# Kernel tuning notes

Hardware: AMD Instinct MI355X
Metric: run time of the kernel (lower is better)

## Reference

```python
import jax, jax.numpy as jnp
import numpy as np

BATCH, IN_F, OUT_F, BASIS = 64, 512, 512, 8


def _cheb_basis(x):
    # Chebyshev basis T_k(tanh(x)) for k=1..BASIS; x: (b, i) -> (b, i, BASIS)
    theta = jnp.arccos(jnp.clip(jnp.tanh(x), -1.0 + 1e-6, 1.0 - 1e-6))
    ks = jnp.arange(1, BASIS + 1, dtype=x.dtype)
    return jnp.cos(theta[..., None] * ks)


def setup_inputs() -> dict:
    key = jax.random.key(0)
    k1, k2, k3 = jax.random.split(key, 3)
    x = jax.random.normal(k1, (BATCH, IN_F), dtype=jnp.float32)
    # xavier_normal_ on w: std = sqrt(2 / (fan_in + fan_out))
    w = jax.random.normal(k2, (IN_F, OUT_F), dtype=jnp.float32) * np.sqrt(2.0 / (IN_F + OUT_F))
    # normal_(c, 0, 0.1)
    c = jax.random.normal(k3, (IN_F, OUT_F, BASIS), dtype=jnp.float32) * 0.1
    return {"x": x, "w": w, "c": c}


def reference(x, w, c):
    # basis: (b, i, k); contract basis dim with c: (i, o, k) -> (b, i, o)
    basis = _cheb_basis(x)
    s = jnp.einsum("bik,iok->bio", basis, c)
    # residual SiLU(x) broadcast over o, weight by w, reduce over in_features
    out = jnp.einsum("bio,io->bo", jax.nn.silu(x)[:, :, None] + s, w)
    return out
```

## Files before the change

kernel.cpp:

```cpp
#include <hip/hip_runtime.h>

#define BATCH 64
#define IN_F 512
#define OUT_F 512
#define ICH 16
#define NKB (IN_F / ICH)
#define NNB 16

typedef short short8 __attribute__((ext_vector_type(8)));
typedef float f32x4 __attribute__((ext_vector_type(4)));

static __device__ __forceinline__ unsigned bfpk(float a, float b) {
    unsigned ua = __float_as_uint(a) + 0x8000u;
    unsigned ub = __float_as_uint(b) + 0x8000u;
    return __builtin_amdgcn_perm(ub, ua, 0x07060302u);
}

__global__ __launch_bounds__(256, 2) void kan_mfma(const float* __restrict__ x,
                                                   const float* __restrict__ w,
                                                   const float* __restrict__ c,
                                                   float* __restrict__ out) {
    __shared__ __align__(16) short T_lds[ICH * BATCH * 8];
    __shared__ __align__(16) short S_lds[BATCH * ICH];

    int nb  = blockIdx.x & (NNB - 1);
    int kb  = blockIdx.x >> 4;
    int i0  = kb * ICH;
    int o0  = nb * 32;
    int tid = threadIdx.x;

    {
        int b  = tid & 63;
        int wq = tid >> 6;
        float4 xv4 = *(const float4*)(x + (size_t)b * IN_F + i0 + wq * 4);
        float xs[4] = {xv4.x, xv4.y, xv4.z, xv4.w};
#pragma unroll
        for (int j = 0; j < 4; ++j) {
            int il = wq * 4 + j;
            float xv = xs[j];
            float xc = fminf(fmaxf(xv, -15.f), 15.f);
            float u  = __expf(-xc);
            float sl = __fdividef(xv, 1.0f + u);
            float u2 = u * u;
            float t  = __fdividef(1.0f - u2, 1.0f + u2);
            t = fminf(fmaxf(t, -1.0f + 1e-6f), 1.0f - 1e-6f);
            float t2 = t + t;
            float T1 = t;
            float T2 = fmaf(t2, T1, -1.0f);
            float T3 = fmaf(t2, T2, -T1);
            float T4 = fmaf(t2, T3, -T2);
            float T5 = fmaf(t2, T4, -T3);
            float T6 = fmaf(t2, T5, -T4);
            float T7 = fmaf(t2, T6, -T5);
            float T8 = fmaf(t2, T7, -T6);
            union { short8 v; unsigned u4[4]; } fr;
            fr.u4[0] = bfpk(T1, T2);
            fr.u4[1] = bfpk(T3, T4);
            fr.u4[2] = bfpk(T5, T6);
            fr.u4[3] = bfpk(T7, T8);
            *(short8*)&T_lds[(il * BATCH + b) * 8] = fr.v;
            S_lds[b * ICH + il] = (short)(bfpk(sl, 0.f) & 0xffffu);
        }
    }
    __syncthreads();

    int lane = tid & 63;
    int wid  = tid >> 6;
    int m    = lane & 15;
    int quad = lane >> 4;
    int oh   = wid & 1;
    int bp   = wid >> 1;
    int o    = o0 + oh * 16 + m;

    short8 af[2][4];
    short8 aw[2];
#pragma unroll
    for (int u = 0; u < 2; ++u) {
        int b = bp * 32 + u * 16 + m;
#pragma unroll
        for (int s = 0; s < 4; ++s)
            af[u][s] = *(const short8*)&T_lds[((s * 4 + quad) * BATCH + b) * 8];
        aw[u] = (quad < 2) ? *(const short8*)&S_lds[b * ICH + quad * 8]
                           : short8{0, 0, 0, 0, 0, 0, 0, 0};
    }

    f32x4 acc0 = {0.f, 0.f, 0.f, 0.f};
    f32x4 acc1 = {0.f, 0.f, 0.f, 0.f};

#pragma unroll
    for (int s = 0; s < 4; ++s) {
        int i = i0 + s * 4 + quad;
        const float4* cp = (const float4*)(c + ((size_t)i * OUT_F + o) * 8);
        float4 c0 = cp[0];
        float4 c1 = cp[1];
        float wv = w[(size_t)i * OUT_F + o];
        union { short8 v; unsigned u4[4]; } bf;
        bf.u4[0] = bfpk(wv * c0.x, wv * c0.y);
        bf.u4[1] = bfpk(wv * c0.z, wv * c0.w);
        bf.u4[2] = bfpk(wv * c1.x, wv * c1.y);
        bf.u4[3] = bfpk(wv * c1.z, wv * c1.w);
        acc0 = __builtin_amdgcn_mfma_f32_16x16x32_bf16(af[0][s], bf.v, acc0, 0, 0, 0);
        acc1 = __builtin_amdgcn_mfma_f32_16x16x32_bf16(af[1][s], bf.v, acc1, 0, 0, 0);
    }

    union { short8 v; unsigned u4[4]; } bw;
    if (quad < 2) {
        const float* wp = w + (size_t)(i0 + quad * 8) * OUT_F + o;
        bw.u4[0] = bfpk(wp[0 * OUT_F], wp[1 * OUT_F]);
        bw.u4[1] = bfpk(wp[2 * OUT_F], wp[3 * OUT_F]);
        bw.u4[2] = bfpk(wp[4 * OUT_F], wp[5 * OUT_F]);
        bw.u4[3] = bfpk(wp[6 * OUT_F], wp[7 * OUT_F]);
    } else {
        bw.u4[0] = bw.u4[1] = bw.u4[2] = bw.u4[3] = 0u;
    }
    acc0 = __builtin_amdgcn_mfma_f32_16x16x32_bf16(aw[0], bw.v, acc0, 0, 0, 0);
    acc1 = __builtin_amdgcn_mfma_f32_16x16x32_bf16(aw[1], bw.v, acc1, 0, 0, 0);

#pragma unroll
    for (int r = 0; r < 4; ++r) {
        atomicAdd(out + (size_t)(bp * 32 + 0 * 16 + quad * 4 + r) * OUT_F + o, acc0[r]);
        atomicAdd(out + (size_t)(bp * 32 + 1 * 16 + quad * 4 + r) * OUT_F + o, acc1[r]);
    }
}

extern "C" void kernel_launch(void* const* d_in, const int* in_sizes, int n_in,
                              void* d_out, int out_size, void* d_ws, size_t ws_size,
                              hipStream_t stream) {
    const float* x = (const float*)d_in[0];
    const float* w = (const float*)d_in[1];
    const float* c = (const float*)d_in[2];
    float* out = (float*)d_out;

    kan_mfma<<<NKB * NNB, 256, 0, stream>>>(x, w, c, out);
}
```

Baseline: 68.25 us.

## Retile KAN MFMA kernel to 32-input chunks and 16-output tiles per block

Each block now covers 32 input features and 16 outputs instead of 16 inputs and 32 outputs. Every wave handles one 16-row batch slice, which halves the atomicAdd count per block and lets the SiLU MFMA use all four quads with no zero padding. The total number of blocks stays the same, but each block evaluates the basis for twice as many inputs, so the transcendental work per output is higher. The SiLU values are also packed into one vector LDS store instead of scalar stores.

Result: faster. 66.11 us (-3.1%).

```diff
diff --git a/kernel.cpp b/kernel.cpp
--- a/kernel.cpp
+++ b/kernel.cpp
@@ -3,9 +3,9 @@
 #define BATCH 64
 #define IN_F 512
 #define OUT_F 512
-#define ICH 16
+#define ICH 32
 #define NKB (IN_F / ICH)
-#define NNB 16
+#define NNB 32
 
 typedef short short8 __attribute__((ext_vector_type(8)));
 typedef float f32x4 __attribute__((ext_vector_type(4)));
@@ -24,19 +24,23 @@
     __shared__ __align__(16) short S_lds[BATCH * ICH];
 
     int nb  = blockIdx.x & (NNB - 1);
-    int kb  = blockIdx.x >> 4;
+    int kb  = blockIdx.x >> 5;
     int i0  = kb * ICH;
-    int o0  = nb * 32;
+    int o0  = nb * 16;
     int tid = threadIdx.x;
 
     {
         int b  = tid & 63;
         int wq = tid >> 6;
-        float4 xv4 = *(const float4*)(x + (size_t)b * IN_F + i0 + wq * 4);
-        float xs[4] = {xv4.x, xv4.y, xv4.z, xv4.w};
+        const float* xp = x + (size_t)b * IN_F + i0 + wq * 8;
+        float4 xa = *(const float4*)xp;
+        float4 xb = *(const float4*)(xp + 4);
+        float xs[8] = {xa.x, xa.y, xa.z, xa.w, xb.x, xb.y, xb.z, xb.w};
+        unsigned spk[4];
+        float sl_prev = 0.f;
 #pragma unroll
-        for (int j = 0; j < 4; ++j) {
-            int il = wq * 4 + j;
+        for (int j = 0; j < 8; ++j) {
+            int il = wq * 8 + j;
             float xv = xs[j];
             float xc = fminf(fmaxf(xv, -15.f), 15.f);
             float u  = __expf(-xc);
@@ -59,8 +63,13 @@
             fr.u4[2] = bfpk(T5, T6);
             fr.u4[3] = bfpk(T7, T8);
             *(short8*)&T_lds[(il * BATCH + b) * 8] = fr.v;
-            S_lds[b * ICH + il] = (short)(bfpk(sl, 0.f) & 0xffffu);
+            if (j & 1) spk[j >> 1] = bfpk(sl_prev, sl);
+            sl_prev = sl;
         }
+        union { short8 v; unsigned u4[4]; } sv;
+        sv.u4[0] = spk[0]; sv.u4[1] = spk[1];
+        sv.u4[2] = spk[2]; sv.u4[3] = spk[3];
+        *(short8*)&S_lds[b * ICH + wq * 8] = sv.v;
     }
     __syncthreads();
 
@@ -68,27 +77,13 @@
     int wid  = tid >> 6;
     int m    = lane & 15;
     int quad = lane >> 4;
-    int oh   = wid & 1;
-    int bp   = wid >> 1;
-    int o    = o0 + oh * 16 + m;
+    int b    = wid * 16 + m;
+    int o    = o0 + m;
 
-    short8 af[2][4];
-    short8 aw[2];
-#pragma unroll
-    for (int u = 0; u < 2; ++u) {
-        int b = bp * 32 + u * 16 + m;
-#pragma unroll
-        for (int s = 0; s < 4; ++s)
-            af[u][s] = *(const short8*)&T_lds[((s * 4 + quad) * BATCH + b) * 8];
-        aw[u] = (quad < 2) ? *(const short8*)&S_lds[b * ICH + quad * 8]
-                           : short8{0, 0, 0, 0, 0, 0, 0, 0};
-    }
-
-    f32x4 acc0 = {0.f, 0.f, 0.f, 0.f};
-    f32x4 acc1 = {0.f, 0.f, 0.f, 0.f};
+    f32x4 acc = {0.f, 0.f, 0.f, 0.f};
 
 #pragma unroll
-    for (int s = 0; s < 4; ++s) {
+    for (int s = 0; s < 8; ++s) {
         int i = i0 + s * 4 + quad;
         const float4* cp = (const float4*)(c + ((size_t)i * OUT_F + o) * 8);
         float4 c0 = cp[0];
@@ -99,28 +94,24 @@
         bf.u4[1] = bfpk(wv * c0.z, wv * c0.w);
         bf.u4[2] = bfpk(wv * c1.x, wv * c1.y);
         bf.u4[3] = bfpk(wv * c1.z, wv * c1.w);
-        acc0 = __builtin_amdgcn_mfma_f32_16x16x32_bf16(af[0][s], bf.v, acc0, 0, 0, 0);
-        acc1 = __builtin_amdgcn_mfma_f32_16x16x32_bf16(af[1][s], bf.v, acc1, 0, 0, 0);
+        short8 af = *(const short8*)&T_lds[((s * 4 + quad) * BATCH + b) * 8];
+        acc = __builtin_amdgcn_mfma_f32_16x16x32_bf16(af, bf.v, acc, 0, 0, 0);
     }
 
-    union { short8 v; unsigned u4[4]; } bw;
-    if (quad < 2) {
+    {
+        short8 aw = *(const short8*)&S_lds[b * ICH + quad * 8];
         const float* wp = w + (size_t)(i0 + quad * 8) * OUT_F + o;
+        union { short8 v; unsigned u4[4]; } bw;
         bw.u4[0] = bfpk(wp[0 * OUT_F], wp[1 * OUT_F]);
         bw.u4[1] = bfpk(wp[2 * OUT_F], wp[3 * OUT_F]);
         bw.u4[2] = bfpk(wp[4 * OUT_F], wp[5 * OUT_F]);
         bw.u4[3] = bfpk(wp[6 * OUT_F], wp[7 * OUT_F]);
-    } else {
-        bw.u4[0] = bw.u4[1] = bw.u4[2] = bw.u4[3] = 0u;
+        acc = __builtin_amdgcn_mfma_f32_16x16x32_bf16(aw, bw.v, acc, 0, 0, 0);
     }
-    acc0 = __builtin_amdgcn_mfma_f32_16x16x32_bf16(aw[0], bw.v, acc0, 0, 0, 0);
-    acc1 = __builtin_amdgcn_mfma_f32_16x16x32_bf16(aw[1], bw.v, acc1, 0, 0, 0);
 
 #pragma unroll
-    for (int r = 0; r < 4; ++r) {
-        atomicAdd(out + (size_t)(bp * 32 + 0 * 16 + quad * 4 + r) * OUT_F + o, acc0[r]);
-        atomicAdd(out + (size_t)(bp * 32 + 1 * 16 + quad * 4 + r) * OUT_F + o, acc1[r]);
-    }
+    for (int r = 0; r < 4; ++r)
+        atomicAdd(out + (size_t)(wid * 16 + quad * 4 + r) * OUT_F + o, acc[r]);
 }
 
 extern "C" void kernel_launch(void* const* d_in, const int* in_sizes, int n_in,
```
